# Performance work log

Measured on AMD Instinct MI355X. Metric: run time of the kernel, lower is better.

Reference implementation:

```python
import jax, jax.numpy as jnp
import numpy as np

B, S, T, H, NH, NL = 16, 128, 64, 128, 8, 4
DH = H // NH
FF = 2 * H
SCALE = 1.0 / float(np.sqrt(DH))


def _ln(x, s, b):
    m = x.mean(-1, keepdims=True)
    v = ((x - m) ** 2).mean(-1, keepdims=True)
    return (x - m) * jax.lax.rsqrt(v + 1e-5) * s + b


def _block(x, mask, p):
    Wq, bq, Wk, bk, Wv, bv, Wo, bo, s1, c1, W1, d1, W2, d2, s2, c2 = p
    N, L, _ = x.shape
    q = (x @ Wq + bq).reshape(N, L, NH, DH)
    k = (x @ Wk + bk).reshape(N, L, NH, DH)
    v = (x @ Wv + bv).reshape(N, L, NH, DH)
    scores = jnp.einsum('nqhd,nkhd->nhqk', q, k) * SCALE
    scores = jnp.where(mask[:, None, :, :], scores, -1e9)
    a = jax.nn.softmax(scores, axis=-1)
    o = jnp.einsum('nhqk,nkhd->nqhd', a, v).reshape(N, L, H)
    x = _ln(x + o @ Wo + bo, s1, c1)
    h = jax.nn.relu(x @ W1 + d1)
    return _ln(x + h @ W2 + d2, s2, c2)


def setup_inputs():
    key = jax.random.key(0)
    ks = jax.random.split(key, 16)
    g = lambda k, shape: jax.random.normal(k, shape, jnp.float32) * 0.02
    return {
        'polylines': jax.random.normal(ks[0], (B, S, T, H), jnp.float32),
        'lengths': jax.random.randint(ks[1], (B, S), 0, T + 1),
        'proj_w': g(ks[2], (H, H)), 'proj_b': jnp.zeros((H,), jnp.float32),
        'proj_ln_s': jnp.ones((H,), jnp.float32), 'proj_ln_b': jnp.zeros((H,), jnp.float32),
        'pos_emb': g(ks[3], (1, T, H)),
        'Wq': g(ks[4], (NL, H, H)), 'bq': jnp.zeros((NL, H), jnp.float32),
        'Wk': g(ks[5], (NL, H, H)), 'bk': jnp.zeros((NL, H), jnp.float32),
        'Wv': g(ks[6], (NL, H, H)), 'bv': jnp.zeros((NL, H), jnp.float32),
        'Wo': g(ks[7], (NL, H, H)), 'bo': jnp.zeros((NL, H), jnp.float32),
        'ln1_s': jnp.ones((NL, H), jnp.float32), 'ln1_b': jnp.zeros((NL, H), jnp.float32),
        'W1': g(ks[8], (NL, H, FF)), 'b1': jnp.zeros((NL, FF), jnp.float32),
        'W2': g(ks[9], (NL, FF, H)), 'b2': jnp.zeros((NL, H), jnp.float32),
        'ln2_s': jnp.ones((NL, H), jnp.float32), 'ln2_b': jnp.zeros((NL, H), jnp.float32),
    }


def reference(polylines, lengths, proj_w, proj_b, proj_ln_s, proj_ln_b, pos_emb,
              Wq, bq, Wk, bk, Wv, bv, Wo, bo, ln1_s, ln1_b, W1, b1, W2, b2, ln2_s, ln2_b):
    # valid[b,s,t] = t < lengths[b,s]; lengths==0 -> polyline absent (fully padded)
    valid = jnp.arange(T)[None, None, :] < lengths[:, :, None]  # [B,S,T]
    x = jnp.where(valid[..., None], polylines, -1.0)            # -1 pad as in np.pad(constant_values=-1)
    # mask_temporal[b,s] = outer(valid[b,s], valid[b,s])
    mask_t = (valid[:, :, :, None] & valid[:, :, None, :]).reshape(B * S, T, T)
    # mask_spatial[b,t] = outer(valid[b,:,t], valid[b,:,t])
    vs = jnp.transpose(valid, (0, 2, 1))                        # [B,T,S]
    mask_s = (vs[:, :, :, None] & vs[:, :, None, :]).reshape(B * T, S, S)

    x = x.reshape(B * S, T, H)
    x = jax.nn.relu(_ln(x @ proj_w + proj_b, proj_ln_s, proj_ln_b))  # MLP: Linear->LN->ReLU
    x = x + pos_emb[:, :T, :]

    mask = mask_t
    for i in range(NL):
        if i == NL // 2:
            # switch from temporal to spatial attention: [B*S,T,H] -> [B*T,S,H]
            x = x.reshape(B, S, T, H).transpose(0, 2, 1, 3).reshape(B * T, S, H)
            mask = mask_s
        p = (Wq[i], bq[i], Wk[i], bk[i], Wv[i], bv[i], Wo[i], bo[i],
             ln1_s[i], ln1_b[i], W1[i], b1[i], W2[i], b2[i], ln2_s[i], ln2_b[i])
        x = _block(x, mask, p)
    # faithful to original final reshape (treats [B*T,S,H] buffer as [B,S,T,H])
    return x.reshape(B, S, T, H)[:, 0, :]
```

## Files before the change

### kernel.cpp

```cpp
#include <hip/hip_runtime.h>

typedef short short8 __attribute__((ext_vector_type(8)));
typedef short short4_t __attribute__((ext_vector_type(4)));
typedef float floatx4 __attribute__((ext_vector_type(4)));
typedef unsigned short ushort_t;

#define B_ 16
#define S_ 128
#define T_ 64
#define H_ 128
#define FF_ 256
#define SCALEQK 0.25f

#define OFFP 0
#define OFFQ(l) (16384 + (l) * 65536)
#define OFFK(l) (OFFQ(l) + 16384)
#define OFFV(l) (OFFQ(l) + 32768)
#define OFFO(l) (OFFQ(l) + 49152)
#define OFFW1(l) (278528 + (l) * 65536)
#define OFFW2(l) (OFFW1(l) + 32768)

__device__ __forceinline__ float b2f(ushort_t u) {
    union { unsigned int i; float f; } x; x.i = ((unsigned int)u) << 16; return x.f;
}
__device__ __forceinline__ ushort_t f2b(float f) {
    union { float f; unsigned int i; } x; x.f = f;
    unsigned int r = x.i + 0x7fffu + ((x.i >> 16) & 1u);
    return (ushort_t)(r >> 16);
}
__device__ __forceinline__ int pack2b(float a, float b) {
    return (int)f2b(a) | ((int)f2b(b) << 16);
}

struct WtEnt { const float* src; int N; int K; int nclog2; int dstoff; };
struct WtArgs { WtEnt e[25]; };

__global__ __launch_bounds__(256) void wt_kernel(WtArgs a, ushort_t* __restrict__ dst) {
    WtEnt ent = a.e[blockIdx.x];
    const int tiles_c = ent.N >> 5;
    const int nt = (ent.K >> 5) * tiles_c;
    const int t = blockIdx.y;
    if (t >= nt) return;
    const int tc = t & (tiles_c - 1);
    const int tr = t >> ent.nclog2;
    __shared__ float ld[32 * 33];
    const int tid = threadIdx.x;
#pragma unroll
    for (int i = 0; i < 4; ++i) {
        int e = tid + i * 256;
        int rr = e >> 5, cc = e & 31;
        ld[rr * 33 + cc] = ent.src[(tr * 32 + rr) * ent.N + tc * 32 + cc];
    }
    __syncthreads();
    ushort_t* d = dst + ent.dstoff;
#pragma unroll
    for (int i = 0; i < 4; ++i) {
        int e = tid + i * 256;
        int rr = e >> 5, cc = e & 31;
        d[(tc * 32 + rr) * ent.K + tr * 32 + cc] = f2b(ld[cc * 33 + rr]);
    }
}

template<int RT, int CT, int KK>
__device__ __forceinline__ void mm_g(const ushort_t* aL, int sa,
                                     const ushort_t* __restrict__ wT,
                                     int colbase, int lane, floatx4 (&acc)[RT][CT]) {
    const int l15 = lane & 15, lq8 = (lane >> 4) * 8;
#pragma unroll
    for (int r = 0; r < RT; ++r)
#pragma unroll
        for (int c = 0; c < CT; ++c) acc[r][c] = (floatx4){0.f, 0.f, 0.f, 0.f};
#pragma unroll
    for (int k0 = 0; k0 < KK; k0 += 32) {
        short8 b[CT];
#pragma unroll
        for (int c = 0; c < CT; ++c)
            b[c] = *(const short8*)&wT[(colbase + c * 16 + l15) * KK + k0 + lq8];
#pragma unroll
        for (int r = 0; r < RT; ++r) {
            short8 a = *(const short8*)&aL[(r * 16 + l15) * sa + k0 + lq8];
#pragma unroll
            for (int c = 0; c < CT; ++c)
                acc[r][c] = __builtin_amdgcn_mfma_f32_16x16x32_bf16(a, b[c], acc[r][c], 0, 0, 0);
        }
    }
}

template<int RT, int CT>
__device__ __forceinline__ void add_bias(floatx4 (&acc)[RT][CT], const float* b,
                                         int colbase, int l15) {
#pragma unroll
    for (int c = 0; c < CT; ++c) {
        float bc = b[colbase + c * 16 + l15];
#pragma unroll
        for (int r = 0; r < RT; ++r)
#pragma unroll
            for (int g = 0; g < 4; ++g) acc[r][c][g] += bc;
    }
}

template<int RT, int CT>
__device__ __forceinline__ void add_resid_reg(floatx4 (&acc)[RT][CT],
                                              const float (&res)[RT][CT][4]) {
#pragma unroll
    for (int r = 0; r < RT; ++r)
#pragma unroll
        for (int c = 0; c < CT; ++c)
#pragma unroll
            for (int g = 0; g < 4; ++g) acc[r][c][g] += res[r][c][g];
}
template<int RT, int CT>
__device__ __forceinline__ void save_resid(float (&res)[RT][CT][4],
                                           const floatx4 (&acc)[RT][CT]) {
#pragma unroll
    for (int r = 0; r < RT; ++r)
#pragma unroll
        for (int c = 0; c < CT; ++c)
#pragma unroll
            for (int g = 0; g < 4; ++g) res[r][c][g] = acc[r][c][g];
}

template<int RT, int CT>
__device__ __forceinline__ void st_n(const floatx4 (&acc)[RT][CT], ushort_t* dst, int stride,
                                     int colbase, int l15, int lq) {
#pragma unroll
    for (int r = 0; r < RT; ++r)
#pragma unroll
        for (int g = 0; g < 4; ++g) {
            int row = r * 16 + lq * 4 + g;
#pragma unroll
            for (int c = 0; c < CT; ++c)
                dst[row * stride + colbase + c * 16 + l15] = f2b(acc[r][c][g]);
        }
}

template<int RT, int CT>
__device__ __forceinline__ void st_t(const floatx4 (&acc)[RT][CT], ushort_t* dst, int stride,
                                     int colbase, int l15, int lq) {
#pragma unroll
    for (int r = 0; r < RT; ++r)
#pragma unroll
        for (int c = 0; c < CT; ++c) {
            int d = colbase + c * 16 + l15;
            short4_t p;
#pragma unroll
            for (int g = 0; g < 4; ++g) p[g] = (short)f2b(acc[r][c][g]);
            *(short4_t*)&dst[d * stride + r * 16 + lq * 4] = p;
        }
}

template<int RT, int CT>
__device__ __forceinline__ void ln_norm(floatx4 (&acc)[RT][CT], float* redL,
                                        const float* lns, const float* lnb,
                                        int colbase, int l15, int lq, int wv) {
#pragma unroll
    for (int r = 0; r < RT; ++r)
#pragma unroll
        for (int g = 0; g < 4; ++g) {
            float s = 0.f, q = 0.f;
#pragma unroll
            for (int c = 0; c < CT; ++c) { float v = acc[r][c][g]; s += v; q += v * v; }
            s += __shfl_xor(s, 1); s += __shfl_xor(s, 2); s += __shfl_xor(s, 4); s += __shfl_xor(s, 8);
            q += __shfl_xor(q, 1); q += __shfl_xor(q, 2); q += __shfl_xor(q, 4); q += __shfl_xor(q, 8);
            if (l15 == 0) {
                int row = r * 16 + lq * 4 + g;
                redL[row * 8 + wv] = s;
                redL[row * 8 + 4 + wv] = q;
            }
        }
    __syncthreads();
#pragma unroll
    for (int r = 0; r < RT; ++r)
#pragma unroll
        for (int g = 0; g < 4; ++g) {
            int row = r * 16 + lq * 4 + g;
            float4 S = *(float4*)&redL[row * 8];
            float4 Q = *(float4*)&redL[row * 8 + 4];
            float mean = (S.x + S.y + S.z + S.w) * (1.f / 128.f);
            float var = (Q.x + Q.y + Q.z + Q.w) * (1.f / 128.f) - mean * mean;
            float rstd = rsqrtf(var + 1e-5f);
#pragma unroll
            for (int c = 0; c < CT; ++c) {
                int col = colbase + c * 16 + l15;
                acc[r][c][g] = (acc[r][c][g] - mean) * rstd * lns[col] + lnb[col];
            }
        }
}

template<int JT>
__device__ __forceinline__ void softmax_pack(floatx4 (&st)[JT], bool iv, unsigned jm,
                                             int (&px)[JT][2]) {
    float ev[JT][4];
    float mx = -3.0e38f;
#pragma unroll
    for (int jt = 0; jt < JT; ++jt)
#pragma unroll
        for (int g = 0; g < 4; ++g) {
            bool ok = iv && ((jm >> (jt * 4 + g)) & 1u);
            float s = ok ? st[jt][g] * SCALEQK : -1e9f;
            ev[jt][g] = s; mx = fmaxf(mx, s);
        }
    mx = fmaxf(mx, __shfl_xor(mx, 16)); mx = fmaxf(mx, __shfl_xor(mx, 32));
    float sum = 0.f;
#pragma unroll
    for (int jt = 0; jt < JT; ++jt)
#pragma unroll
        for (int g = 0; g < 4; ++g) { float e = __expf(ev[jt][g] - mx); ev[jt][g] = e; sum += e; }
    sum += __shfl_xor(sum, 16); sum += __shfl_xor(sum, 32);
    float inv = 1.f / sum;
#pragma unroll
    for (int jt = 0; jt < JT; ++jt) {
        px[jt][0] = pack2b(ev[jt][0] * inv, ev[jt][1] * inv);
        px[jt][1] = pack2b(ev[jt][2] * inv, ev[jt][3] * inv);
    }
}

__device__ __forceinline__ short8 pfrag(const int (*px)[2], int jc, int lq, int l15) {
    const int jA = (lq & 1) * 32 + l15;
    int a0 = __shfl(px[jc * 2][0], jA);
    int a1 = __shfl(px[jc * 2][1], jA);
    int a2 = __shfl(px[jc * 2][0], jA + 16);
    int a3 = __shfl(px[jc * 2][1], jA + 16);
    int b0 = __shfl(px[jc * 2 + 1][0], jA);
    int b1 = __shfl(px[jc * 2 + 1][1], jA);
    int b2 = __shfl(px[jc * 2 + 1][0], jA + 16);
    int b3 = __shfl(px[jc * 2 + 1][1], jA + 16);
    const bool t = (lq >> 1) != 0;
    union { int4 i; short8 s; } u;
    u.i = make_int4(t ? b0 : a0, t ? b1 : a1, t ? b2 : a2, t ? b3 : a3);
    return u.s;
}
__device__ __forceinline__ short8 vfrag(const ushort_t* vT, int stride, int row, int off) {
    int2 a = *(const int2*)&vT[row * stride + off];
    int2 b = *(const int2*)&vT[row * stride + off + 4];
    union { int4 i; short8 s; } u;
    u.i = make_int4(a.x, a.y, b.x, b.y);
    return u.s;
}

__global__ __launch_bounds__(256, 2) void k1_mega(
    const float* __restrict__ poly, const int* __restrict__ lens,
    const ushort_t* __restrict__ wt,
    const float* __restrict__ projb, const float* __restrict__ pls,
    const float* __restrict__ plb, const float* __restrict__ pos,
    const float* __restrict__ bq0, const float* __restrict__ bk0,
    const float* __restrict__ bv0, const float* __restrict__ bo0,
    const float* __restrict__ l1s0, const float* __restrict__ l1b0,
    const float* __restrict__ b10, const float* __restrict__ b20,
    const float* __restrict__ l2s0, const float* __restrict__ l2b0,
    const float* __restrict__ bq1, const float* __restrict__ bk1,
    const float* __restrict__ bv1,
    ushort_t* __restrict__ o1, float* __restrict__ xr0f)
{
    __shared__ ushort_t pool[34816];
    __shared__ float redL[512];
    __shared__ float psL[8 * 68];
    __shared__ float q1L[128];
    ushort_t* xL = pool;
    ushort_t* qL = pool + 8704;
    ushort_t* kL = pool + 17408;
    ushort_t* vT = pool + 26112;
    ushort_t* hL = pool + 17408;

    const int tid = threadIdx.x, lane = tid & 63, wv = tid >> 6;
    const int l15 = lane & 15, lq = lane >> 4;
    const int gid = blockIdx.x;
    const int len = lens[gid];

    {
        const float* pg = poly + (size_t)gid * 8192;
#pragma unroll
        for (int it = 0; it < 8; ++it) {
            int e4 = (tid + it * 256) * 4;
            int row = e4 >> 7, col = e4 & 127;
            float4 f = *(const float4*)(pg + e4);
            if (row >= len) { f.x = -1.f; f.y = -1.f; f.z = -1.f; f.w = -1.f; }
            short4_t u;
            u[0] = (short)f2b(f.x); u[1] = (short)f2b(f.y);
            u[2] = (short)f2b(f.z); u[3] = (short)f2b(f.w);
            *(short4_t*)&xL[row * 136 + col] = u;
        }
    }
    __syncthreads();

    floatx4 a2[4][2];
    float xre[4][2][4];

    mm_g<4, 2, 128>(xL, 136, wt + OFFP, wv * 32, lane, a2);
    add_bias<4, 2>(a2, projb, wv * 32, l15);
    ln_norm<4, 2>(a2, redL, pls, plb, wv * 32, l15, lq, wv);
    __syncthreads();
#pragma unroll
    for (int r = 0; r < 4; ++r)
#pragma unroll
        for (int gg = 0; gg < 4; ++gg) {
            int row = r * 16 + lq * 4 + gg;
#pragma unroll
            for (int c = 0; c < 2; ++c) {
                int col = wv * 32 + c * 16 + l15;
                float v = fmaxf(a2[r][c][gg], 0.f) + pos[row * 128 + col];
                xre[r][c][gg] = v;
                xL[row * 136 + col] = f2b(v);
            }
        }
    __syncthreads();

    mm_g<4, 2, 128>(xL, 136, wt + OFFQ(0), wv * 32, lane, a2);
    add_bias<4, 2>(a2, bq0, wv * 32, l15);
    st_n<4, 2>(a2, qL, 136, wv * 32, l15, lq);
    mm_g<4, 2, 128>(xL, 136, wt + OFFK(0), wv * 32, lane, a2);
    add_bias<4, 2>(a2, bk0, wv * 32, l15);
    st_n<4, 2>(a2, kL, 136, wv * 32, l15, lq);
    mm_g<4, 2, 128>(xL, 136, wt + OFFV(0), wv * 32, lane, a2);
    add_bias<4, 2>(a2, bv0, wv * 32, l15);
    st_t<4, 2>(a2, vT, 68, wv * 32, l15, lq);
    __syncthreads();

    {
        const int iRow = wv * 16 + l15;
        const bool iv = iRow < len;
        unsigned jm = 0;
#pragma unroll
        for (int jt = 0; jt < 4; ++jt)
#pragma unroll
            for (int gg = 0; gg < 4; ++gg)
                if (jt * 16 + lq * 4 + gg < len) jm |= (1u << (jt * 4 + gg));
        for (int h = 0; h < 8; ++h) {
            const int hc = h * 16;
            short8 z8 = {0, 0, 0, 0, 0, 0, 0, 0};
            short8 bqf = z8;
            if (lq < 2) bqf = *(const short8*)&qL[iRow * 136 + hc + lq * 8];
            floatx4 st[4];
#pragma unroll
            for (int jt = 0; jt < 4; ++jt) {
                short8 ak = z8;
                if (lq < 2) ak = *(const short8*)&kL[(jt * 16 + l15) * 136 + hc + lq * 8];
                floatx4 zz = {0.f, 0.f, 0.f, 0.f};
                st[jt] = __builtin_amdgcn_mfma_f32_16x16x32_bf16(ak, bqf, zz, 0, 0, 0);
            }
            int px[4][2];
            softmax_pack<4>(st, iv, jm, px);
            floatx4 ao = {0.f, 0.f, 0.f, 0.f};
#pragma unroll
            for (int jc = 0; jc < 2; ++jc) {
                short8 av = vfrag(vT, 68, hc + l15, jc * 32 + lq * 8);
                short8 bp = pfrag(px, jc, lq, l15);
                ao = __builtin_amdgcn_mfma_f32_16x16x32_bf16(av, bp, ao, 0, 0, 0);
            }
            short4_t w;
#pragma unroll
            for (int gg = 0; gg < 4; ++gg) w[gg] = (short)f2b(ao[gg]);
            *(short4_t*)&qL[iRow * 136 + hc + lq * 4] = w;
        }
    }
    __syncthreads();

    mm_g<4, 2, 128>(qL, 136, wt + OFFO(0), wv * 32, lane, a2);
    add_bias<4, 2>(a2, bo0, wv * 32, l15);
    add_resid_reg<4, 2>(a2, xre);
    ln_norm<4, 2>(a2, redL, l1s0, l1b0, wv * 32, l15, lq, wv);
    save_resid<4, 2>(xre, a2);
    st_n<4, 2>(a2, xL, 136, wv * 32, l15, lq);
    __syncthreads();

    {
        floatx4 a4[4][4];
        mm_g<4, 4, 128>(xL, 136, wt + OFFW1(0), wv * 64, lane, a4);
        add_bias<4, 4>(a4, b10, wv * 64, l15);
#pragma unroll
        for (int r = 0; r < 4; ++r)
#pragma unroll
            for (int c = 0; c < 4; ++c)
#pragma unroll
                for (int gg = 0; gg < 4; ++gg) a4[r][c][gg] = fmaxf(a4[r][c][gg], 0.f);
        st_n<4, 4>(a4, hL, 272, wv * 64, l15, lq);
    }
    __syncthreads();

    mm_g<4, 2, 256>(hL, 272, wt + OFFW2(0), wv * 32, lane, a2);
    add_bias<4, 2>(a2, b20, wv * 32, l15);
    add_resid_reg<4, 2>(a2, xre);
    ln_norm<4, 2>(a2, redL, l2s0, l2b0, wv * 32, l15, lq, wv);
    save_resid<4, 2>(xre, a2);
    st_n<4, 2>(a2, xL, 136, wv * 32, l15, lq);
    if (lq == 0) {
#pragma unroll
        for (int c = 0; c < 2; ++c)
            xr0f[(size_t)gid * 128 + wv * 32 + c * 16 + l15] = a2[0][c][0];
    }
    __syncthreads();

    mm_g<4, 2, 128>(xL, 136, wt + OFFK(1), wv * 32, lane, a2);
    add_bias<4, 2>(a2, bk1, wv * 32, l15);
    st_n<4, 2>(a2, kL, 136, wv * 32, l15, lq);
    mm_g<4, 2, 128>(xL, 136, wt + OFFV(1), wv * 32, lane, a2);
    add_bias<4, 2>(a2, bv1, wv * 32, l15);
    st_t<4, 2>(a2, vT, 68, wv * 32, l15, lq);
    if (tid < 128) {
        int d = tid;
        float a = bq1[d];
        const ushort_t* wq = wt + OFFQ(1) + d * 128;
#pragma unroll 4
        for (int j0 = 0; j0 < 128; j0 += 8) {
            short8 w8 = *(const short8*)&wq[j0];
            short8 x8 = *(const short8*)&xL[j0];
#pragma unroll
            for (int q = 0; q < 8; ++q)
                a = fmaf(b2f((ushort_t)x8[q]), b2f((ushort_t)w8[q]), a);
        }
        q1L[d] = a;
    }
    __syncthreads();

    {
        int h = tid >> 5, jj = tid & 31;
        int hc = h * 16;
        float s[2];
#pragma unroll
        for (int half = 0; half < 2; ++half) {
            int j = jj + half * 32;
            float a = 0.f;
            short8 k0v = *(const short8*)&kL[j * 136 + hc];
            short8 k1v = *(const short8*)&kL[j * 136 + hc + 8];
#pragma unroll
            for (int q = 0; q < 8; ++q) {
                a = fmaf(q1L[hc + q], b2f((ushort_t)k0v[q]), a);
                a = fmaf(q1L[hc + 8 + q], b2f((ushort_t)k1v[q]), a);
            }
            s[half] = (j < len) ? a * SCALEQK : -1e9f;
        }
        float mx = fmaxf(s[0], s[1]);
#pragma unroll
        for (int d = 1; d < 32; d <<= 1) mx = fmaxf(mx, __shfl_xor(mx, d));
        float e0 = __expf(s[0] - mx), e1 = __expf(s[1] - mx);
        float sum = e0 + e1;
#pragma unroll
        for (int d = 1; d < 32; d <<= 1) sum += __shfl_xor(sum, d);
        float inv = 1.f / sum;
        psL[h * 68 + jj] = e0 * inv;
        psL[h * 68 + jj + 32] = e1 * inv;
    }
    __syncthreads();
    if (tid < 128) {
        int h = tid >> 4, d = tid & 15, hc = h * 16;
        float a = 0.f;
#pragma unroll 4
        for (int j0 = 0; j0 < 64; j0 += 4) {
            float4 p4 = *(const float4*)&psL[h * 68 + j0];
            short4_t v4 = *(const short4_t*)&vT[(hc + d) * 68 + j0];
            a += p4.x * b2f((ushort_t)v4[0]) + p4.y * b2f((ushort_t)v4[1])
               + p4.z * b2f((ushort_t)v4[2]) + p4.w * b2f((ushort_t)v4[3]);
        }
        o1[(size_t)gid * 128 + hc + d] = f2b(a);
    }
}

__global__ __launch_bounds__(256, 3) void k2a(
    const ushort_t* __restrict__ xg, const int* __restrict__ lens,
    const ushort_t* __restrict__ wt, int l,
    const float* __restrict__ bq, const float* __restrict__ bk,
    const float* __restrict__ bv,
    ushort_t* __restrict__ aob)
{
    __shared__ ushort_t xL[128 * 136];
    __shared__ ushort_t qL[128 * 24];
    __shared__ ushort_t kL[128 * 24];
    __shared__ ushort_t vT[16 * 136];
    __shared__ int vldL[128];

    const int tid = threadIdx.x, lane = tid & 63, wv = tid >> 6;
    const int l15 = lane & 15, lq = lane >> 4;
    const int g = blockIdx.x, h = blockIdx.y, hc = h * 16;
    const size_t rowg = (size_t)g * 128;

#pragma unroll
    for (int it = 0; it < 8; ++it) {
        int e8 = tid + it * 256;
        int row = e8 >> 4, kg = e8 & 15;
        *(short8*)&xL[row * 136 + kg * 8] = *(const short8*)&xg[(rowg + row) * 128 + kg * 8];
    }
    if (tid < 128) vldL[tid] = (lens[g * 128 + tid] > 0) ? 1 : 0;
    __syncthreads();

    unsigned jm = 0;
#pragma unroll
    for (int jt = 0; jt < 8; ++jt)
#pragma unroll
        for (int gg = 0; gg < 4; ++gg)
            if (vldL[jt * 16 + lq * 4 + gg]) jm |= (1u << (jt * 4 + gg));

    {
        floatx4 a1[2][1];
        mm_g<2, 1, 128>(xL + (wv * 32) * 136, 136, wt + OFFQ(l), hc, lane, a1);
        add_bias<2, 1>(a1, bq, hc, l15);
        st_n<2, 1>(a1, qL + (wv * 32) * 24, 24, 0, l15, lq);
        mm_g<2, 1, 128>(xL + (wv * 32) * 136, 136, wt + OFFK(l), hc, lane, a1);
        add_bias<2, 1>(a1, bk, hc, l15);
        st_n<2, 1>(a1, kL + (wv * 32) * 24, 24, 0, l15, lq);
        mm_g<2, 1, 128>(xL + (wv * 32) * 136, 136, wt + OFFV(l), hc, lane, a1);
        add_bias<2, 1>(a1, bv, hc, l15);
        st_t<2, 1>(a1, vT + wv * 32, 136, 0, l15, lq);
    }
    __syncthreads();

    for (int u = 0; u < 2; ++u) {
        const int iRow = wv * 32 + u * 16 + l15;
        const bool iv = vldL[iRow] != 0;
        short8 z8 = {0, 0, 0, 0, 0, 0, 0, 0};
        short8 bqf = z8;
        if (lq < 2) bqf = *(const short8*)&qL[iRow * 24 + lq * 8];
        floatx4 st[8];
#pragma unroll
        for (int jt = 0; jt < 8; ++jt) {
            short8 ak = z8;
            if (lq < 2) ak = *(const short8*)&kL[(jt * 16 + l15) * 24 + lq * 8];
            floatx4 zz = {0.f, 0.f, 0.f, 0.f};
            st[jt] = __builtin_amdgcn_mfma_f32_16x16x32_bf16(ak, bqf, zz, 0, 0, 0);
        }
        int px[8][2];
        softmax_pack<8>(st, iv, jm, px);
        floatx4 ao = {0.f, 0.f, 0.f, 0.f};
#pragma unroll
        for (int jc = 0; jc < 4; ++jc) {
            short8 av = vfrag(vT, 136, l15, jc * 32 + lq * 8);
            short8 bp = pfrag(px, jc, lq, l15);
            ao = __builtin_amdgcn_mfma_f32_16x16x32_bf16(av, bp, ao, 0, 0, 0);
        }
        short4_t w;
#pragma unroll
        for (int gg = 0; gg < 4; ++gg) w[gg] = (short)f2b(ao[gg]);
        *(short4_t*)&aob[(rowg + iRow) * 128 + hc + lq * 4] = w;
    }
}

template<bool FINAL>
__global__ __launch_bounds__(256, 2) void k2b(
    const ushort_t* __restrict__ ain, float* __restrict__ xr,
    const ushort_t* __restrict__ wt, int l,
    const float* __restrict__ bo_l, const float* __restrict__ l1s_l,
    const float* __restrict__ l1b_l, const float* __restrict__ b1_l,
    const float* __restrict__ b2_l, const float* __restrict__ l2s_l,
    const float* __restrict__ l2b_l,
    ushort_t* __restrict__ xg, float* __restrict__ outp)
{
    __shared__ ushort_t aL[64 * 136];
    __shared__ ushort_t hL[64 * 272];
    __shared__ float redL[512];

    const int tid = threadIdx.x, lane = tid & 63, wv = tid >> 6;
    const int l15 = lane & 15, lq = lane >> 4;
    const size_t rowbase = (size_t)blockIdx.x * (FINAL ? 128 : 64);

#pragma unroll
    for (int it = 0; it < 4; ++it) {
        int e8 = tid + it * 256;
        int row = e8 >> 4, kg = e8 & 15;
        *(short8*)&aL[row * 136 + kg * 8] = *(const short8*)&ain[(rowbase + row) * 128 + kg * 8];
    }
    __syncthreads();

    floatx4 a2[4][2];
    float xre[4][2][4];

    mm_g<4, 2, 128>(aL, 136, wt + OFFO(l), wv * 32, lane, a2);
    add_bias<4, 2>(a2, bo_l, wv * 32, l15);
#pragma unroll
    for (int r = 0; r < 4; ++r)
#pragma unroll
        for (int c = 0; c < 2; ++c)
#pragma unroll
            for (int gg = 0; gg < 4; ++gg)
                a2[r][c][gg] += xr[(rowbase + r * 16 + lq * 4 + gg) * 128 + wv * 32 + c * 16 + l15];
    ln_norm<4, 2>(a2, redL, l1s_l, l1b_l, wv * 32, l15, lq, wv);
    save_resid<4, 2>(xre, a2);
    st_n<4, 2>(a2, aL, 136, wv * 32, l15, lq);
    __syncthreads();

    {
        floatx4 a4[4][4];
        mm_g<4, 4, 128>(aL, 136, wt + OFFW1(l), wv * 64, lane, a4);
        add_bias<4, 4>(a4, b1_l, wv * 64, l15);
#pragma unroll
        for (int r = 0; r < 4; ++r)
#pragma unroll
            for (int c = 0; c < 4; ++c)
#pragma unroll
                for (int gg = 0; gg < 4; ++gg) a4[r][c][gg] = fmaxf(a4[r][c][gg], 0.f);
        st_n<4, 4>(a4, hL, 272, wv * 64, l15, lq);
    }
    __syncthreads();

    mm_g<4, 2, 256>(hL, 272, wt + OFFW2(l), wv * 32, lane, a2);
    add_bias<4, 2>(a2, b2_l, wv * 32, l15);
    add_resid_reg<4, 2>(a2, xre);
    ln_norm<4, 2>(a2, redL, l2s_l, l2b_l, wv * 32, l15, lq, wv);

    if (FINAL) {
#pragma unroll
        for (int r = 0; r < 4; ++r)
#pragma unroll
            for (int c = 0; c < 2; ++c)
#pragma unroll
                for (int gg = 0; gg < 4; ++gg) {
                    int row = r * 16 + lq * 4 + gg;
                    outp[((size_t)(blockIdx.x * 64 + row)) * 128 + wv * 32 + c * 16 + l15] =
                        a2[r][c][gg];
                }
    } else {
#pragma unroll
        for (int r = 0; r < 4; ++r)
#pragma unroll
            for (int c = 0; c < 2; ++c)
#pragma unroll
                for (int gg = 0; gg < 4; ++gg) {
                    size_t grow = rowbase + r * 16 + lq * 4 + gg;
                    int col = wv * 32 + c * 16 + l15;
                    float v = a2[r][c][gg];
                    xg[grow * 128 + col] = f2b(v);
                    xr[grow * 128 + col] = v;
                }
    }
}

extern "C" void kernel_launch(void* const* d_in, const int* in_sizes, int n_in,
                              void* d_out, int out_size, void* d_ws, size_t ws_size,
                              hipStream_t stream)
{
    const float* poly   = (const float*)d_in[0];
    const int*   lens   = (const int*)d_in[1];
    const float* proj_w = (const float*)d_in[2];
    const float* proj_b = (const float*)d_in[3];
    const float* pls    = (const float*)d_in[4];
    const float* plb    = (const float*)d_in[5];
    const float* pos    = (const float*)d_in[6];
    const float* Wq = (const float*)d_in[7];
    const float* bq = (const float*)d_in[8];
    const float* Wk = (const float*)d_in[9];
    const float* bk = (const float*)d_in[10];
    const float* Wv = (const float*)d_in[11];
    const float* bv = (const float*)d_in[12];
    const float* Wo = (const float*)d_in[13];
    const float* bo = (const float*)d_in[14];
    const float* l1s = (const float*)d_in[15];
    const float* l1b = (const float*)d_in[16];
    const float* W1 = (const float*)d_in[17];
    const float* b1 = (const float*)d_in[18];
    const float* W2 = (const float*)d_in[19];
    const float* b2 = (const float*)d_in[20];
    const float* l2s = (const float*)d_in[21];
    const float* l2b = (const float*)d_in[22];
    float* outp = (float*)d_out;

    char* base = (char*)d_ws;
    ushort_t* wt    = (ushort_t*)base;
    ushort_t* o1buf = (ushort_t*)(base + 1081344);
    float* xr0f     = (float*)(base + 1605632);
    ushort_t* xgbuf = (ushort_t*)(base + 2654208);
    ushort_t* aob   = (ushort_t*)(base + 3178496);

    const int HH = H_ * H_, HF = H_ * FF_;
    WtArgs wa;
    wa.e[0] = {proj_w, 128, 128, 2, OFFP};
    for (int l = 0; l < 4; ++l) {
        wa.e[1 + l * 4 + 0] = {Wq + l * HH, 128, 128, 2, OFFQ(l)};
        wa.e[1 + l * 4 + 1] = {Wk + l * HH, 128, 128, 2, OFFK(l)};
        wa.e[1 + l * 4 + 2] = {Wv + l * HH, 128, 128, 2, OFFV(l)};
        wa.e[1 + l * 4 + 3] = {Wo + l * HH, 128, 128, 2, OFFO(l)};
    }
    for (int l = 0; l < 4; ++l) {
        wa.e[17 + l * 2 + 0] = {W1 + l * HF, 256, 128, 3, OFFW1(l)};
        wa.e[17 + l * 2 + 1] = {W2 + l * HF, 128, 256, 2, OFFW2(l)};
    }
    wt_kernel<<<dim3(25, 32), 256, 0, stream>>>(wa, wt);

    k1_mega<<<dim3(2048), 256, 0, stream>>>(
        poly, lens, wt,
        proj_b, pls, plb, pos,
        bq, bk, bv, bo, l1s, l1b, b1, b2, l2s, l2b,
        bq + H_, bk + H_, bv + H_,
        o1buf, xr0f);

    k2b<false><<<dim3(32), 256, 0, stream>>>(
        o1buf, xr0f, wt, 1,
        bo + H_, l1s + H_, l1b + H_, b1 + FF_, b2 + H_, l2s + H_, l2b + H_,
        xgbuf, nullptr);
    k2a<<<dim3(16, 8), 256, 0, stream>>>(
        xgbuf, lens, wt, 2, bq + 2 * H_, bk + 2 * H_, bv + 2 * H_, aob);
    k2b<false><<<dim3(32), 256, 0, stream>>>(
        aob, xr0f, wt, 2,
        bo + 2 * H_, l1s + 2 * H_, l1b + 2 * H_, b1 + 2 * FF_, b2 + 2 * H_,
        l2s + 2 * H_, l2b + 2 * H_,
        xgbuf, nullptr);
    k2a<<<dim3(16, 8), 256, 0, stream>>>(
        xgbuf, lens, wt, 3, bq + 3 * H_, bk + 3 * H_, bv + 3 * H_, aob);
    k2b<true><<<dim3(16), 256, 0, stream>>>(
        aob, xr0f, wt, 3,
        bo + 3 * H_, l1s + 3 * H_, l1b + 3 * H_, b1 + 3 * FF_, b2 + 3 * H_,
        l2s + 3 * H_, l2b + 3 * H_,
        nullptr, outp);
}
```

Baseline: 385.5 us.

## Fuse layer-1 row tail into k1_mega and split k2b into smaller row tiles

Moves the layer-1 output projection, first LayerNorm, FFN and second LayerNorm for the single needed row into the tail of k1_mega. This is done with per-thread bf16 dot products, which removes a separate k2b launch and the global round-trip of o1 and xr0f. k2b now processes 16 rows per block instead of 64 or 128, launching 4x more blocks with higher occupancy bounds to fill more CUs. Dot-product loops gain multiple accumulators for ILP. The risks are extra register and LDS pressure in the already large k1_mega, and weights reloaded per block in k2b.

```diff
diff --git a/kernel.cpp b/kernel.cpp
--- a/kernel.cpp
+++ b/kernel.cpp
@@ -249,13 +249,21 @@
     const float* __restrict__ b10, const float* __restrict__ b20,
     const float* __restrict__ l2s0, const float* __restrict__ l2b0,
     const float* __restrict__ bq1, const float* __restrict__ bk1,
-    const float* __restrict__ bv1,
-    ushort_t* __restrict__ o1, float* __restrict__ xr0f)
+    const float* __restrict__ bv1, const float* __restrict__ bo1,
+    const float* __restrict__ l1s1, const float* __restrict__ l1b1,
+    const float* __restrict__ b11, const float* __restrict__ b21,
+    const float* __restrict__ l2s1, const float* __restrict__ l2b1,
+    ushort_t* __restrict__ xg, float* __restrict__ xrf)
 {
     __shared__ ushort_t pool[34816];
     __shared__ float redL[512];
     __shared__ float psL[8 * 68];
     __shared__ float q1L[128];
+    __shared__ ushort_t o1R[128];
+    __shared__ ushort_t y16[128];
+    __shared__ ushort_t h16[256];
+    __shared__ float xr0L[128];
+    __shared__ float lnS[8];
     ushort_t* xL = pool;
     ushort_t* qL = pool + 8704;
     ushort_t* kL = pool + 17408;
@@ -325,6 +333,7 @@
 #pragma unroll
             for (int gg = 0; gg < 4; ++gg)
                 if (jt * 16 + lq * 4 + gg < len) jm |= (1u << (jt * 4 + gg));
+#pragma unroll 2
         for (int h = 0; h < 8; ++h) {
             const int hc = h * 16;
             short8 z8 = {0, 0, 0, 0, 0, 0, 0, 0};
@@ -386,7 +395,7 @@
     if (lq == 0) {
 #pragma unroll
         for (int c = 0; c < 2; ++c)
-            xr0f[(size_t)gid * 128 + wv * 32 + c * 16 + l15] = a2[0][c][0];
+            xr0L[wv * 32 + c * 16 + l15] = a2[0][c][0];
     }
     __syncthreads();
 
@@ -398,17 +407,23 @@
     st_t<4, 2>(a2, vT, 68, wv * 32, l15, lq);
     if (tid < 128) {
         int d = tid;
-        float a = bq1[d];
+        float p0 = 0.f, p1 = 0.f, p2 = 0.f, p3 = 0.f;
         const ushort_t* wq = wt + OFFQ(1) + d * 128;
-#pragma unroll 4
-        for (int j0 = 0; j0 < 128; j0 += 8) {
-            short8 w8 = *(const short8*)&wq[j0];
-            short8 x8 = *(const short8*)&xL[j0];
-#pragma unroll
-            for (int q = 0; q < 8; ++q)
-                a = fmaf(b2f((ushort_t)x8[q]), b2f((ushort_t)w8[q]), a);
-        }
-        q1L[d] = a;
+#pragma unroll
+        for (int j0 = 0; j0 < 128; j0 += 32) {
+            short8 wa = *(const short8*)&wq[j0];      short8 xa = *(const short8*)&xL[j0];
+            short8 wb = *(const short8*)&wq[j0 + 8];  short8 xb = *(const short8*)&xL[j0 + 8];
+            short8 wc = *(const short8*)&wq[j0 + 16]; short8 xc = *(const short8*)&xL[j0 + 16];
+            short8 wd = *(const short8*)&wq[j0 + 24]; short8 xd = *(const short8*)&xL[j0 + 24];
+#pragma unroll
+            for (int q = 0; q < 8; ++q) {
+                p0 = fmaf(b2f((ushort_t)xa[q]), b2f((ushort_t)wa[q]), p0);
+                p1 = fmaf(b2f((ushort_t)xb[q]), b2f((ushort_t)wb[q]), p1);
+                p2 = fmaf(b2f((ushort_t)xc[q]), b2f((ushort_t)wc[q]), p2);
+                p3 = fmaf(b2f((ushort_t)xd[q]), b2f((ushort_t)wd[q]), p3);
+            }
+        }
+        q1L[d] = bq1[d] + ((p0 + p1) + (p2 + p3));
     }
     __syncthreads();
 
@@ -419,15 +434,15 @@
 #pragma unroll
         for (int half = 0; half < 2; ++half) {
             int j = jj + half * 32;
-            float a = 0.f;
+            float a0 = 0.f, a1 = 0.f;
             short8 k0v = *(const short8*)&kL[j * 136 + hc];
             short8 k1v = *(const short8*)&kL[j * 136 + hc + 8];
 #pragma unroll
             for (int q = 0; q < 8; ++q) {
-                a = fmaf(q1L[hc + q], b2f((ushort_t)k0v[q]), a);
-                a = fmaf(q1L[hc + 8 + q], b2f((ushort_t)k1v[q]), a);
-            }
-            s[half] = (j < len) ? a * SCALEQK : -1e9f;
+                a0 = fmaf(q1L[hc + q], b2f((ushort_t)k0v[q]), a0);
+                a1 = fmaf(q1L[hc + 8 + q], b2f((ushort_t)k1v[q]), a1);
+            }
+            s[half] = (j < len) ? (a0 + a1) * SCALEQK : -1e9f;
         }
         float mx = fmaxf(s[0], s[1]);
 #pragma unroll
@@ -443,15 +458,107 @@
     __syncthreads();
     if (tid < 128) {
         int h = tid >> 4, d = tid & 15, hc = h * 16;
-        float a = 0.f;
-#pragma unroll 4
-        for (int j0 = 0; j0 < 64; j0 += 4) {
-            float4 p4 = *(const float4*)&psL[h * 68 + j0];
-            short4_t v4 = *(const short4_t*)&vT[(hc + d) * 68 + j0];
-            a += p4.x * b2f((ushort_t)v4[0]) + p4.y * b2f((ushort_t)v4[1])
-               + p4.z * b2f((ushort_t)v4[2]) + p4.w * b2f((ushort_t)v4[3]);
-        }
-        o1[(size_t)gid * 128 + hc + d] = f2b(a);
+        float a0 = 0.f, a1 = 0.f;
+#pragma unroll
+        for (int j0 = 0; j0 < 64; j0 += 8) {
+            float4 pa = *(const float4*)&psL[h * 68 + j0];
+            float4 pb = *(const float4*)&psL[h * 68 + j0 + 4];
+            short4_t va = *(const short4_t*)&vT[(hc + d) * 68 + j0];
+            short4_t vb = *(const short4_t*)&vT[(hc + d) * 68 + j0 + 4];
+            a0 += pa.x * b2f((ushort_t)va[0]) + pa.y * b2f((ushort_t)va[1])
+                + pa.z * b2f((ushort_t)va[2]) + pa.w * b2f((ushort_t)va[3]);
+            a1 += pb.x * b2f((ushort_t)vb[0]) + pb.y * b2f((ushort_t)vb[1])
+                + pb.z * b2f((ushort_t)vb[2]) + pb.w * b2f((ushort_t)vb[3]);
+        }
+        o1R[tid] = f2b(a0 + a1);
+    }
+    __syncthreads();
+
+    float yv = 0.f, yln = 0.f, ov = 0.f;
+    if (tid < 128) {
+        float p0 = 0.f, p1 = 0.f, p2 = 0.f, p3 = 0.f;
+        const ushort_t* wo = wt + OFFO(1) + tid * 128;
+#pragma unroll
+        for (int j0 = 0; j0 < 128; j0 += 32) {
+            short8 wa = *(const short8*)&wo[j0];      short8 xa = *(const short8*)&o1R[j0];
+            short8 wb = *(const short8*)&wo[j0 + 8];  short8 xb = *(const short8*)&o1R[j0 + 8];
+            short8 wc = *(const short8*)&wo[j0 + 16]; short8 xc = *(const short8*)&o1R[j0 + 16];
+            short8 wd = *(const short8*)&wo[j0 + 24]; short8 xd = *(const short8*)&o1R[j0 + 24];
+#pragma unroll
+            for (int q = 0; q < 8; ++q) {
+                p0 = fmaf(b2f((ushort_t)xa[q]), b2f((ushort_t)wa[q]), p0);
+                p1 = fmaf(b2f((ushort_t)xb[q]), b2f((ushort_t)wb[q]), p1);
+                p2 = fmaf(b2f((ushort_t)xc[q]), b2f((ushort_t)wc[q]), p2);
+                p3 = fmaf(b2f((ushort_t)xd[q]), b2f((ushort_t)wd[q]), p3);
+            }
+        }
+        yv = bo1[tid] + ((p0 + p1) + (p2 + p3)) + xr0L[tid];
+        float s = yv, qq = yv * yv;
+#pragma unroll
+        for (int d = 1; d < 32; d <<= 1) { s += __shfl_xor(s, d); qq += __shfl_xor(qq, d); }
+        if (lane == 0) { lnS[wv] = s; lnS[4 + wv] = qq; }
+    }
+    __syncthreads();
+    if (tid < 128) {
+        float mean = (lnS[0] + lnS[1]) * (1.f / 128.f);
+        float var = (lnS[4] + lnS[5]) * (1.f / 128.f) - mean * mean;
+        float rstd = rsqrtf(var + 1e-5f);
+        yln = (yv - mean) * rstd * l1s1[tid] + l1b1[tid];
+        y16[tid] = f2b(yln);
+    }
+    __syncthreads();
+    {
+        float p0 = 0.f, p1 = 0.f, p2 = 0.f, p3 = 0.f;
+        const ushort_t* w1 = wt + OFFW1(1) + tid * 128;
+#pragma unroll
+        for (int j0 = 0; j0 < 128; j0 += 32) {
+            short8 wa = *(const short8*)&w1[j0];      short8 xa = *(const short8*)&y16[j0];
+            short8 wb = *(const short8*)&w1[j0 + 8];  short8 xb = *(const short8*)&y16[j0 + 8];
+            short8 wc = *(const short8*)&w1[j0 + 16]; short8 xc = *(const short8*)&y16[j0 + 16];
+            short8 wd = *(const short8*)&w1[j0 + 24]; short8 xd = *(const short8*)&y16[j0 + 24];
+#pragma unroll
+            for (int q = 0; q < 8; ++q) {
+                p0 = fmaf(b2f((ushort_t)xa[q]), b2f((ushort_t)wa[q]), p0);
+                p1 = fmaf(b2f((ushort_t)xb[q]), b2f((ushort_t)wb[q]), p1);
+                p2 = fmaf(b2f((ushort_t)xc[q]), b2f((ushort_t)wc[q]), p2);
+                p3 = fmaf(b2f((ushort_t)xd[q]), b2f((ushort_t)wd[q]), p3);
+            }
+        }
+        float h = b11[tid] + ((p0 + p1) + (p2 + p3));
+        h16[tid] = f2b(fmaxf(h, 0.f));
+    }
+    __syncthreads();
+    if (tid < 128) {
+        float p0 = 0.f, p1 = 0.f, p2 = 0.f, p3 = 0.f;
+        const ushort_t* w2 = wt + OFFW2(1) + tid * 256;
+#pragma unroll
+        for (int j0 = 0; j0 < 256; j0 += 32) {
+            short8 wa = *(const short8*)&w2[j0];      short8 xa = *(const short8*)&h16[j0];
+            short8 wb = *(const short8*)&w2[j0 + 8];  short8 xb = *(const short8*)&h16[j0 + 8];
+            short8 wc = *(const short8*)&w2[j0 + 16]; short8 xc = *(const short8*)&h16[j0 + 16];
+            short8 wd = *(const short8*)&w2[j0 + 24]; short8 xd = *(const short8*)&h16[j0 + 24];
+#pragma unroll
+            for (int q = 0; q < 8; ++q) {
+                p0 = fmaf(b2f((ushort_t)xa[q]), b2f((ushort_t)wa[q]), p0);
+                p1 = fmaf(b2f((ushort_t)xb[q]), b2f((ushort_t)wb[q]), p1);
+                p2 = fmaf(b2f((ushort_t)xc[q]), b2f((ushort_t)wc[q]), p2);
+                p3 = fmaf(b2f((ushort_t)xd[q]), b2f((ushort_t)wd[q]), p3);
+            }
+        }
+        ov = b21[tid] + ((p0 + p1) + (p2 + p3)) + yln;
+        float s = ov, qq = ov * ov;
+#pragma unroll
+        for (int d = 1; d < 32; d <<= 1) { s += __shfl_xor(s, d); qq += __shfl_xor(qq, d); }
+        if (lane == 0) { lnS[wv] = s; lnS[4 + wv] = qq; }
+    }
+    __syncthreads();
+    if (tid < 128) {
+        float mean = (lnS[0] + lnS[1]) * (1.f / 128.f);
+        float var = (lnS[4] + lnS[5]) * (1.f / 128.f) - mean * mean;
+        float rstd = rsqrtf(var + 1e-5f);
+        float oln = (ov - mean) * rstd * l2s1[tid] + l2b1[tid];
+        xg[(size_t)gid * 128 + tid] = f2b(oln);
+        xrf[(size_t)gid * 128 + tid] = oln;
     }
 }
 
@@ -534,7 +641,7 @@
 }
 
 template<bool FINAL>
-__global__ __launch_bounds__(256, 2) void k2b(
+__global__ __launch_bounds__(256, 4) void k2b(
     const ushort_t* __restrict__ ain, float* __restrict__ xr,
     const ushort_t* __restrict__ wt, int l,
     const float* __restrict__ bo_l, const float* __restrict__ l1s_l,
@@ -543,82 +650,73 @@
     const float* __restrict__ l2b_l,
     ushort_t* __restrict__ xg, float* __restrict__ outp)
 {
-    __shared__ ushort_t aL[64 * 136];
-    __shared__ ushort_t hL[64 * 272];
-    __shared__ float redL[512];
+    __shared__ ushort_t aL[16 * 136];
+    __shared__ ushort_t hL[16 * 272];
+    __shared__ float redL[128];
 
     const int tid = threadIdx.x, lane = tid & 63, wv = tid >> 6;
     const int l15 = lane & 15, lq = lane >> 4;
-    const size_t rowbase = (size_t)blockIdx.x * (FINAL ? 128 : 64);
-
-#pragma unroll
-    for (int it = 0; it < 4; ++it) {
-        int e8 = tid + it * 256;
-        int row = e8 >> 4, kg = e8 & 15;
+    const int blk = blockIdx.x;
+    const size_t rowbase = FINAL ? ((size_t)(blk >> 2) * 128 + (blk & 3) * 16)
+                                 : ((size_t)blk * 16);
+
+    {
+        int row = tid >> 4, kg = tid & 15;
         *(short8*)&aL[row * 136 + kg * 8] = *(const short8*)&ain[(rowbase + row) * 128 + kg * 8];
     }
     __syncthreads();
 
-    floatx4 a2[4][2];
-    float xre[4][2][4];
-
-    mm_g<4, 2, 128>(aL, 136, wt + OFFO(l), wv * 32, lane, a2);
-    add_bias<4, 2>(a2, bo_l, wv * 32, l15);
-#pragma unroll
-    for (int r = 0; r < 4; ++r)
+    floatx4 a2[1][2];
+    float xre[1][2][4];
+
+    mm_g<1, 2, 128>(aL, 136, wt + OFFO(l), wv * 32, lane, a2);
+    add_bias<1, 2>(a2, bo_l, wv * 32, l15);
+#pragma unroll
+    for (int c = 0; c < 2; ++c)
+#pragma unroll
+        for (int gg = 0; gg < 4; ++gg)
+            a2[0][c][gg] += xr[(rowbase + lq * 4 + gg) * 128 + wv * 32 + c * 16 + l15];
+    ln_norm<1, 2>(a2, redL, l1s_l, l1b_l, wv * 32, l15, lq, wv);
+    save_resid<1, 2>(xre, a2);
+    st_n<1, 2>(a2, aL, 136, wv * 32, l15, lq);
+    __syncthreads();
+
+    {
+        floatx4 a4[1][4];
+        mm_g<1, 4, 128>(aL, 136, wt + OFFW1(l), wv * 64, lane, a4);
+        add_bias<1, 4>(a4, b1_l, wv * 64, l15);
+#pragma unroll
+        for (int c = 0; c < 4; ++c)
+#pragma unroll
+            for (int gg = 0; gg < 4; ++gg) a4[0][c][gg] = fmaxf(a4[0][c][gg], 0.f);
+        st_n<1, 4>(a4, hL, 272, wv * 64, l15, lq);
+    }
+    __syncthreads();
+
+    mm_g<1, 2, 256>(hL, 272, wt + OFFW2(l), wv * 32, lane, a2);
+    add_bias<1, 2>(a2, b2_l, wv * 32, l15);
+    add_resid_reg<1, 2>(a2, xre);
+    ln_norm<1, 2>(a2, redL, l2s_l, l2b_l, wv * 32, l15, lq, wv);
+
+    if (FINAL) {
 #pragma unroll
         for (int c = 0; c < 2; ++c)
 #pragma unroll
-            for (int gg = 0; gg < 4; ++gg)
-                a2[r][c][gg] += xr[(rowbase + r * 16 + lq * 4 + gg) * 128 + wv * 32 + c * 16 + l15];
-    ln_norm<4, 2>(a2, redL, l1s_l, l1b_l, wv * 32, l15, lq, wv);
-    save_resid<4, 2>(xre, a2);
-    st_n<4, 2>(a2, aL, 136, wv * 32, l15, lq);
-    __syncthreads();
-
-    {
-        floatx4 a4[4][4];
-        mm_g<4, 4, 128>(aL, 136, wt + OFFW1(l), wv * 64, lane, a4);
-        add_bias<4, 4>(a4, b1_l, wv * 64, l15);
-#pragma unroll
-        for (int r = 0; r < 4; ++r)
-#pragma unroll
-            for (int c = 0; c < 4; ++c)
-#pragma unroll
-                for (int gg = 0; gg < 4; ++gg) a4[r][c][gg] = fmaxf(a4[r][c][gg], 0.f);
-        st_n<4, 4>(a4, hL, 272, wv * 64, l15, lq);
-    }
-    __syncthreads();
-
-    mm_g<4, 2, 256>(hL, 272, wt + OFFW2(l), wv * 32, lane, a2);
-    add_bias<4, 2>(a2, b2_l, wv * 32, l15);
-    add_resid_reg<4, 2>(a2, xre);
-    ln_norm<4, 2>(a2, redL, l2s_l, l2b_l, wv * 32, l15, lq, wv);
-
-    if (FINAL) {
-#pragma unroll
-        for (int r = 0; r < 4; ++r)
-#pragma unroll
-            for (int c = 0; c < 2; ++c)
-#pragma unroll
-                for (int gg = 0; gg < 4; ++gg) {
-                    int row = r * 16 + lq * 4 + gg;
-                    outp[((size_t)(blockIdx.x * 64 + row)) * 128 + wv * 32 + c * 16 + l15] =
-                        a2[r][c][gg];
-                }
+            for (int gg = 0; gg < 4; ++gg) {
+                int orow = (blk >> 2) * 64 + (blk & 3) * 16 + lq * 4 + gg;
+                outp[(size_t)orow * 128 + wv * 32 + c * 16 + l15] = a2[0][c][gg];
+            }
     } else {
 #pragma unroll
-        for (int r = 0; r < 4; ++r)
-#pragma unroll
-            for (int c = 0; c < 2; ++c)
-#pragma unroll
-                for (int gg = 0; gg < 4; ++gg) {
-                    size_t grow = rowbase + r * 16 + lq * 4 + gg;
-                    int col = wv * 32 + c * 16 + l15;
-                    float v = a2[r][c][gg];
-                    xg[grow * 128 + col] = f2b(v);
-                    xr[grow * 128 + col] = v;
-                }
+        for (int c = 0; c < 2; ++c)
+#pragma unroll
+            for (int gg = 0; gg < 4; ++gg) {
+                size_t grow = rowbase + lq * 4 + gg;
+                int col = wv * 32 + c * 16 + l15;
+                float v = a2[0][c][gg];
+                xg[grow * 128 + col] = f2b(v);
+                xr[grow * 128 + col] = v;
+            }
     }
 }
 
@@ -653,10 +751,9 @@
 
     char* base = (char*)d_ws;
     ushort_t* wt    = (ushort_t*)base;
-    ushort_t* o1buf = (ushort_t*)(base + 1081344);
-    float* xr0f     = (float*)(base + 1605632);
-    ushort_t* xgbuf = (ushort_t*)(base + 2654208);
-    ushort_t* aob   = (ushort_t*)(base + 3178496);
+    ushort_t* xgbuf = (ushort_t*)(base + 1081344);
+    float* xrf      = (float*)(base + 1605632);
+    ushort_t* aob   = (ushort_t*)(base + 2654208);
 
     const int HH = H_ * H_, HF = H_ * FF_;
     WtArgs wa;
@@ -677,24 +774,21 @@
         poly, lens, wt,
         proj_b, pls, plb, pos,
         bq, bk, bv, bo, l1s, l1b, b1, b2, l2s, l2b,
-        bq + H_, bk + H_, bv + H_,
-        o1buf, xr0f);
-
-    k2b<false><<<dim3(32), 256, 0, stream>>>(
-        o1buf, xr0f, wt, 1,
-        bo + H_, l1s + H_, l1b + H_, b1 + FF_, b2 + H_, l2s + H_, l2b + H_,
-        xgbuf, nullptr);
+        bq + H_, bk + H_, bv + H_, bo + H_,
+        l1s + H_, l1b + H_, b1 + FF_, b2 + H_, l2s + H_, l2b + H_,
+        xgbuf, xrf);
+
     k2a<<<dim3(16, 8), 256, 0, stream>>>(
         xgbuf, lens, wt, 2, bq + 2 * H_, bk + 2 * H_, bv + 2 * H_, aob);
-    k2b<false><<<dim3(32), 256, 0, stream>>>(
-        aob, xr0f, wt, 2,
+    k2b<false><<<dim3(128), 256, 0, stream>>>(
+        aob, xrf, wt, 2,
         bo + 2 * H_, l1s + 2 * H_, l1b + 2 * H_, b1 + 2 * FF_, b2 + 2 * H_,
         l2s + 2 * H_, l2b + 2 * H_,
         xgbuf, nullptr);
     k2a<<<dim3(16, 8), 256, 0, stream>>>(
         xgbuf, lens, wt, 3, bq + 3 * H_, bk + 3 * H_, bv + 3 * H_, aob);
-    k2b<true><<<dim3(16), 256, 0, stream>>>(
-        aob, xr0f, wt, 3,
+    k2b<true><<<dim3(64), 256, 0, stream>>>(
+        aob, xrf, wt, 3,
         bo + 3 * H_, l1s + 3 * H_, l1b + 3 * H_, b1 + 3 * FF_, b2 + 3 * H_,
         l2s + 3 * H_, l2b + 3 * H_,
         nullptr, outp);
```

Result: no change. 388.4 us (+0.7%).

## Fuse tail layers into one cooperative kernel with grid syncs

Applied to the files above, without the earlier changes.

The five tail launches (FFN and spatial-attention stages for layers 1-3) become a single cooperative kernel of 128 blocks. Grid-wide syncs separate the stages and all stages share one static shared-memory buffer. The FFN stage is retiled from 64-row blocks (32 blocks) to 16-row blocks (128 blocks), so more CUs work on it and the launch gaps between small kernels go away. In exchange it adds grid-sync cost, lowers per-block MFMA reuse of weights, and forces occupancy to one block per CU.

```diff
diff --git a/kernel.cpp b/kernel.cpp
--- a/kernel.cpp
+++ b/kernel.cpp
@@ -1,4 +1,7 @@
 #include <hip/hip_runtime.h>
+#include <hip/hip_cooperative_groups.h>
+
+namespace cg = cooperative_groups;
 
 typedef short short8 __attribute__((ext_vector_type(8)));
 typedef short short4_t __attribute__((ext_vector_type(4)));
@@ -455,22 +458,22 @@
     }
 }
 
-__global__ __launch_bounds__(256, 3) void k2a(
+__device__ __forceinline__ void k2a_body(char* smem, int blk,
     const ushort_t* __restrict__ xg, const int* __restrict__ lens,
     const ushort_t* __restrict__ wt, int l,
     const float* __restrict__ bq, const float* __restrict__ bk,
     const float* __restrict__ bv,
     ushort_t* __restrict__ aob)
 {
-    __shared__ ushort_t xL[128 * 136];
-    __shared__ ushort_t qL[128 * 24];
-    __shared__ ushort_t kL[128 * 24];
-    __shared__ ushort_t vT[16 * 136];
-    __shared__ int vldL[128];
+    ushort_t* xL = (ushort_t*)(smem);
+    ushort_t* qL = (ushort_t*)(smem + 34816);
+    ushort_t* kL = (ushort_t*)(smem + 40960);
+    ushort_t* vT = (ushort_t*)(smem + 47104);
+    int* vldL = (int*)(smem + 51456);
 
     const int tid = threadIdx.x, lane = tid & 63, wv = tid >> 6;
     const int l15 = lane & 15, lq = lane >> 4;
-    const int g = blockIdx.x, h = blockIdx.y, hc = h * 16;
+    const int g = blk >> 3, h = blk & 7, hc = h * 16;
     const size_t rowg = (size_t)g * 128;
 
 #pragma unroll
@@ -534,92 +537,115 @@
 }
 
 template<bool FINAL>
-__global__ __launch_bounds__(256, 2) void k2b(
+__device__ __forceinline__ void k2b_body(char* smem, int blk,
     const ushort_t* __restrict__ ain, float* __restrict__ xr,
     const ushort_t* __restrict__ wt, int l,
-    const float* __restrict__ bo_l, const float* __restrict__ l1s_l,
-    const float* __restrict__ l1b_l, const float* __restrict__ b1_l,
-    const float* __restrict__ b2_l, const float* __restrict__ l2s_l,
-    const float* __restrict__ l2b_l,
+    const float* bo_l, const float* l1s_l, const float* l1b_l,
+    const float* b1_l, const float* b2_l, const float* l2s_l, const float* l2b_l,
     ushort_t* __restrict__ xg, float* __restrict__ outp)
 {
-    __shared__ ushort_t aL[64 * 136];
-    __shared__ ushort_t hL[64 * 272];
-    __shared__ float redL[512];
+    ushort_t* aL = (ushort_t*)(smem);
+    ushort_t* hL = (ushort_t*)(smem + 4352);
+    float* redL = (float*)(smem + 13056);
 
     const int tid = threadIdx.x, lane = tid & 63, wv = tid >> 6;
     const int l15 = lane & 15, lq = lane >> 4;
-    const size_t rowbase = (size_t)blockIdx.x * (FINAL ? 128 : 64);
-
-#pragma unroll
-    for (int it = 0; it < 4; ++it) {
-        int e8 = tid + it * 256;
-        int row = e8 >> 4, kg = e8 & 15;
+    const size_t rowbase = FINAL ? ((size_t)(blk >> 2) * 128 + (blk & 3) * 16)
+                                 : ((size_t)blk * 16);
+
+    {
+        int row = tid >> 4, kg = tid & 15;
         *(short8*)&aL[row * 136 + kg * 8] = *(const short8*)&ain[(rowbase + row) * 128 + kg * 8];
     }
     __syncthreads();
 
-    floatx4 a2[4][2];
-    float xre[4][2][4];
-
-    mm_g<4, 2, 128>(aL, 136, wt + OFFO(l), wv * 32, lane, a2);
-    add_bias<4, 2>(a2, bo_l, wv * 32, l15);
-#pragma unroll
-    for (int r = 0; r < 4; ++r)
+    floatx4 a2[1][2];
+    float xre[1][2][4];
+
+    mm_g<1, 2, 128>(aL, 136, wt + OFFO(l), wv * 32, lane, a2);
+    add_bias<1, 2>(a2, bo_l, wv * 32, l15);
+#pragma unroll
+    for (int c = 0; c < 2; ++c)
+#pragma unroll
+        for (int gg = 0; gg < 4; ++gg)
+            a2[0][c][gg] += xr[(rowbase + lq * 4 + gg) * 128 + wv * 32 + c * 16 + l15];
+    ln_norm<1, 2>(a2, redL, l1s_l, l1b_l, wv * 32, l15, lq, wv);
+    save_resid<1, 2>(xre, a2);
+    st_n<1, 2>(a2, aL, 136, wv * 32, l15, lq);
+    __syncthreads();
+
+    {
+        floatx4 a4[1][4];
+        mm_g<1, 4, 128>(aL, 136, wt + OFFW1(l), wv * 64, lane, a4);
+        add_bias<1, 4>(a4, b1_l, wv * 64, l15);
+#pragma unroll
+        for (int c = 0; c < 4; ++c)
+#pragma unroll
+            for (int gg = 0; gg < 4; ++gg) a4[0][c][gg] = fmaxf(a4[0][c][gg], 0.f);
+        st_n<1, 4>(a4, hL, 272, wv * 64, l15, lq);
+    }
+    __syncthreads();
+
+    mm_g<1, 2, 256>(hL, 272, wt + OFFW2(l), wv * 32, lane, a2);
+    add_bias<1, 2>(a2, b2_l, wv * 32, l15);
+    add_resid_reg<1, 2>(a2, xre);
+    ln_norm<1, 2>(a2, redL, l2s_l, l2b_l, wv * 32, l15, lq, wv);
+
+    if (FINAL) {
 #pragma unroll
         for (int c = 0; c < 2; ++c)
 #pragma unroll
-            for (int gg = 0; gg < 4; ++gg)
-                a2[r][c][gg] += xr[(rowbase + r * 16 + lq * 4 + gg) * 128 + wv * 32 + c * 16 + l15];
-    ln_norm<4, 2>(a2, redL, l1s_l, l1b_l, wv * 32, l15, lq, wv);
-    save_resid<4, 2>(xre, a2);
-    st_n<4, 2>(a2, aL, 136, wv * 32, l15, lq);
-    __syncthreads();
-
-    {
-        floatx4 a4[4][4];
-        mm_g<4, 4, 128>(aL, 136, wt + OFFW1(l), wv * 64, lane, a4);
-        add_bias<4, 4>(a4, b1_l, wv * 64, l15);
-#pragma unroll
-        for (int r = 0; r < 4; ++r)
-#pragma unroll
-            for (int c = 0; c < 4; ++c)
-#pragma unroll
-                for (int gg = 0; gg < 4; ++gg) a4[r][c][gg] = fmaxf(a4[r][c][gg], 0.f);
-        st_n<4, 4>(a4, hL, 272, wv * 64, l15, lq);
-    }
-    __syncthreads();
-
-    mm_g<4, 2, 256>(hL, 272, wt + OFFW2(l), wv * 32, lane, a2);
-    add_bias<4, 2>(a2, b2_l, wv * 32, l15);
-    add_resid_reg<4, 2>(a2, xre);
-    ln_norm<4, 2>(a2, redL, l2s_l, l2b_l, wv * 32, l15, lq, wv);
-
-    if (FINAL) {
-#pragma unroll
-        for (int r = 0; r < 4; ++r)
-#pragma unroll
-            for (int c = 0; c < 2; ++c)
-#pragma unroll
-                for (int gg = 0; gg < 4; ++gg) {
-                    int row = r * 16 + lq * 4 + gg;
-                    outp[((size_t)(blockIdx.x * 64 + row)) * 128 + wv * 32 + c * 16 + l15] =
-                        a2[r][c][gg];
-                }
+            for (int gg = 0; gg < 4; ++gg) {
+                int orow = (blk >> 2) * 64 + (blk & 3) * 16 + lq * 4 + gg;
+                outp[(size_t)orow * 128 + wv * 32 + c * 16 + l15] = a2[0][c][gg];
+            }
     } else {
 #pragma unroll
-        for (int r = 0; r < 4; ++r)
-#pragma unroll
-            for (int c = 0; c < 2; ++c)
-#pragma unroll
-                for (int gg = 0; gg < 4; ++gg) {
-                    size_t grow = rowbase + r * 16 + lq * 4 + gg;
-                    int col = wv * 32 + c * 16 + l15;
-                    float v = a2[r][c][gg];
-                    xg[grow * 128 + col] = f2b(v);
-                    xr[grow * 128 + col] = v;
-                }
-    }
+        for (int c = 0; c < 2; ++c)
+#pragma unroll
+            for (int gg = 0; gg < 4; ++gg) {
+                size_t grow = rowbase + lq * 4 + gg;
+                int col = wv * 32 + c * 16 + l15;
+                float v = a2[0][c][gg];
+                xg[grow * 128 + col] = f2b(v);
+                xr[grow * 128 + col] = v;
+            }
+    }
+}
+
+__global__ __launch_bounds__(256, 1) void k2_coop(
+    const ushort_t* __restrict__ o1buf, float* __restrict__ xrf,
+    const int* __restrict__ lens, const ushort_t* __restrict__ wt,
+    const float* __restrict__ bq, const float* __restrict__ bk,
+    const float* __restrict__ bv, const float* __restrict__ bo,
+    const float* __restrict__ l1s, const float* __restrict__ l1b,
+    const float* __restrict__ b1, const float* __restrict__ b2,
+    const float* __restrict__ l2s, const float* __restrict__ l2b,
+    ushort_t* __restrict__ xg, ushort_t* __restrict__ aob,
+    float* __restrict__ outp)
+{
+    cg::grid_group grid = cg::this_grid();
+    __shared__ __align__(16) char smem[51968];
+    const int blk = blockIdx.x;
+
+    k2b_body<false>(smem, blk, o1buf, xrf, wt, 1,
+                    bo + H_, l1s + H_, l1b + H_, b1 + FF_, b2 + H_, l2s + H_, l2b + H_,
+                    xg, nullptr);
+    grid.sync();
+    k2a_body(smem, blk, xg, lens, wt, 2, bq + 2 * H_, bk + 2 * H_, bv + 2 * H_, aob);
+    grid.sync();
+    k2b_body<false>(smem, blk, aob, xrf, wt, 2,
+                    bo + 2 * H_, l1s + 2 * H_, l1b + 2 * H_, b1 + 2 * FF_, b2 + 2 * H_,
+                    l2s + 2 * H_, l2b + 2 * H_,
+                    xg, nullptr);
+    grid.sync();
+    k2a_body(smem, blk, xg, lens, wt, 3, bq + 3 * H_, bk + 3 * H_, bv + 3 * H_, aob);
+    grid.sync();
+    if (blk < 64)
+        k2b_body<true>(smem, blk, aob, xrf, wt, 3,
+                       bo + 3 * H_, l1s + 3 * H_, l1b + 3 * H_, b1 + 3 * FF_, b2 + 3 * H_,
+                       l2s + 3 * H_, l2b + 3 * H_,
+                       nullptr, outp);
 }
 
 extern "C" void kernel_launch(void* const* d_in, const int* in_sizes, int n_in,
@@ -654,7 +680,7 @@
     char* base = (char*)d_ws;
     ushort_t* wt    = (ushort_t*)base;
     ushort_t* o1buf = (ushort_t*)(base + 1081344);
-    float* xr0f     = (float*)(base + 1605632);
+    float* xrf      = (float*)(base + 1605632);
     ushort_t* xgbuf = (ushort_t*)(base + 2654208);
     ushort_t* aob   = (ushort_t*)(base + 3178496);
 
@@ -678,24 +704,19 @@
         proj_b, pls, plb, pos,
         bq, bk, bv, bo, l1s, l1b, b1, b2, l2s, l2b,
         bq + H_, bk + H_, bv + H_,
-        o1buf, xr0f);
-
-    k2b<false><<<dim3(32), 256, 0, stream>>>(
-        o1buf, xr0f, wt, 1,
-        bo + H_, l1s + H_, l1b + H_, b1 + FF_, b2 + H_, l2s + H_, l2b + H_,
-        xgbuf, nullptr);
-    k2a<<<dim3(16, 8), 256, 0, stream>>>(
-        xgbuf, lens, wt, 2, bq + 2 * H_, bk + 2 * H_, bv + 2 * H_, aob);
-    k2b<false><<<dim3(32), 256, 0, stream>>>(
-        aob, xr0f, wt, 2,
-        bo + 2 * H_, l1s + 2 * H_, l1b + 2 * H_, b1 + 2 * FF_, b2 + 2 * H_,
-        l2s + 2 * H_, l2b + 2 * H_,
-        xgbuf, nullptr);
-    k2a<<<dim3(16, 8), 256, 0, stream>>>(
-        xgbuf, lens, wt, 3, bq + 3 * H_, bk + 3 * H_, bv + 3 * H_, aob);
-    k2b<true><<<dim3(16), 256, 0, stream>>>(
-        aob, xr0f, wt, 3,
-        bo + 3 * H_, l1s + 3 * H_, l1b + 3 * H_, b1 + 3 * FF_, b2 + 3 * H_,
-        l2s + 3 * H_, l2b + 3 * H_,
-        nullptr, outp);
-}
+        o1buf, xrf);
+
+    {
+        const ushort_t* p0 = o1buf; float* p1 = xrf; const int* p2 = lens;
+        const ushort_t* p3 = wt;
+        const float* p4 = bq; const float* p5 = bk; const float* p6 = bv;
+        const float* p7 = bo; const float* p8 = l1s; const float* p9 = l1b;
+        const float* p10 = b1; const float* p11 = b2; const float* p12 = l2s;
+        const float* p13 = l2b;
+        ushort_t* p14 = xgbuf; ushort_t* p15 = aob; float* p16 = outp;
+        void* kargs[] = {&p0, &p1, &p2, &p3, &p4, &p5, &p6, &p7, &p8, &p9,
+                         &p10, &p11, &p12, &p13, &p14, &p15, &p16};
+        hipLaunchCooperativeKernel((void*)k2_coop, dim3(128), dim3(256),
+                                   kargs, 0, stream);
+    }
+}
```

Measured after the change: 451.6 us. 17.1% more time.
